# Performance work log

Measured on AMD Instinct MI355X. Metric: run time of the kernel, lower is better.

Reference implementation:

```python
import jax, jax.numpy as jnp
import numpy as np

N_NODES = 50000
N_EDGES = 800000
IN_FEATS = 128
OUT_FEATS = 128


def setup_inputs() -> dict:
    key = jax.random.key(0)
    k1, k2, k3, k4, k5, k6 = jax.random.split(key, 6)
    features = jax.random.normal(k1, (N_NODES, IN_FEATS), dtype=jnp.float32)
    norm = jax.random.uniform(k2, (N_NODES, 1), dtype=jnp.float32)
    W = jax.random.normal(k3, (OUT_FEATS, IN_FEATS), dtype=jnp.float32) * (1.0 / np.sqrt(IN_FEATS))
    b = jax.random.normal(k4, (OUT_FEATS,), dtype=jnp.float32) * 0.01
    src = jax.random.randint(k5, (N_EDGES,), 0, N_NODES, dtype=jnp.int32)
    dst = jax.random.randint(k6, (N_EDGES,), 0, N_NODES, dtype=jnp.int32)
    return {"features": features, "norm": norm, "W": W, "b": b, "src": src, "dst": dst}


def reference(features, norm, W, b, src, dst):
    # message: h_src * norm_src  -> [E, F]
    msg = features[src] * norm[src]
    # reduce: sum over incoming edges, scale by dst norm -> [N, F]
    agg = jax.ops.segment_sum(msg, dst, num_segments=N_NODES) * norm
    # node apply: linear + tanh
    h = jnp.tanh(agg @ W.T + b)
    return h
```

## Files before the change

### kernel.cpp

```cpp
#include <hip/hip_runtime.h>
#include <hip/hip_fp16.h>
#include <math.h>

#define NBITS 7
#define BNODES 128
#define CHUNK 4096
#define BSHIFT 12

typedef _Float16 half4v __attribute__((ext_vector_type(4)));
typedef _Float16 half8v __attribute__((ext_vector_type(8)));
typedef float f32x4 __attribute__((ext_vector_type(4)));

__device__ __forceinline__ unsigned hpack(float a, float b) {
  __half2 h = __floats2half2_rn(a, b);
  return *reinterpret_cast<unsigned*>(&h);
}

union FusedSmem {
  struct {
    _Float16 Wh[128][136];
    _Float16 Ah[64][136];
  } g;
  struct {
    int lcount[512];
    int lbase[512];
    int gbase[512];
    int aux[256];
    unsigned stage[CHUNK];
    int s_total;
  } p;
};

__global__ __launch_bounds__(256) void fused_kernel(
    const float* __restrict__ feat, const float* __restrict__ norm,
    const float* __restrict__ W, unsigned* __restrict__ Yh, int n_nodes,
    const int* __restrict__ src, const int* __restrict__ dst,
    int* __restrict__ cursor, unsigned* __restrict__ recs, int n_edges,
    int nb, int gblocks) {
  __shared__ __align__(16) FusedSmem sm;
  const int t = threadIdx.x;

  if ((int)blockIdx.x < gblocks) {
    const int node0 = blockIdx.x * 64;

#pragma unroll
    for (int k = 0; k < 16; ++k) {
      int e4 = k * 256 + t;
      int oo = e4 >> 5;
      int f4 = (e4 & 31) * 4;
      float4 w = *(const float4*)&W[oo * 128 + f4];
      half4v h;
      h.x = (_Float16)w.x; h.y = (_Float16)w.y;
      h.z = (_Float16)w.z; h.w = (_Float16)w.w;
      *(half4v*)&sm.g.Wh[oo][f4] = h;
    }
#pragma unroll
    for (int k = 0; k < 8; ++k) {
      int e4 = k * 256 + t;
      int nn = e4 >> 5;
      int f4 = (e4 & 31) * 4;
      int node = node0 + nn;
      float4 a = (node < n_nodes)
                     ? *(const float4*)&feat[(size_t)node * 128 + f4]
                     : make_float4(0.f, 0.f, 0.f, 0.f);
      half4v h;
      h.x = (_Float16)a.x; h.y = (_Float16)a.y;
      h.z = (_Float16)a.z; h.w = (_Float16)a.w;
      *(half4v*)&sm.g.Ah[nn][f4] = h;
    }
    __syncthreads();

    const int wv = t >> 6;
    const int l = t & 63;
    const int row16 = l & 15;
    const int kq = l >> 4;

    f32x4 acc[8];
#pragma unroll
    for (int ot = 0; ot < 8; ++ot) acc[ot] = (f32x4){0.f, 0.f, 0.f, 0.f};

#pragma unroll
    for (int ks = 0; ks < 4; ++ks) {
      half8v nfrag = *(const half8v*)&sm.g.Ah[wv * 16 + row16][kq * 8 + ks * 32];
#pragma unroll
      for (int ot = 0; ot < 8; ++ot) {
        half8v wfrag = *(const half8v*)&sm.g.Wh[ot * 16 + row16][kq * 8 + ks * 32];
        acc[ot] = __builtin_amdgcn_mfma_f32_16x16x32_f16(wfrag, nfrag, acc[ot], 0, 0, 0);
      }
    }

    int node = node0 + wv * 16 + row16;
    if (node < n_nodes) {
      float nm = norm[node];
#pragma unroll
      for (int ot = 0; ot < 8; ++ot) {
        uint2 u;
        u.x = hpack(acc[ot][0] * nm, acc[ot][1] * nm);
        u.y = hpack(acc[ot][2] * nm, acc[ot][3] * nm);
        ((uint2*)Yh)[(size_t)node * 32 + ot * 4 + kq] = u;
      }
    }
  } else {
    const int cbase = ((int)blockIdx.x - gblocks) * CHUNK;

    sm.p.lcount[t] = 0; sm.p.lcount[t + 256] = 0;
    __syncthreads();

    int es[16], ed[16], rk[16];
#pragma unroll
    for (int q = 0; q < 4; ++q) {
      int i4 = (cbase >> 2) + q * 256 + t;
      int e0 = i4 << 2;
      int4 sv, dv;
      if (e0 + 3 < n_edges) {
        sv = ((const int4*)src)[i4];
        dv = ((const int4*)dst)[i4];
      } else {
        sv.x = (e0 + 0 < n_edges) ? src[e0 + 0] : 0;
        sv.y = (e0 + 1 < n_edges) ? src[e0 + 1] : 0;
        sv.z = (e0 + 2 < n_edges) ? src[e0 + 2] : 0;
        sv.w = 0;
        dv.x = (e0 + 0 < n_edges) ? dst[e0 + 0] : -1;
        dv.y = (e0 + 1 < n_edges) ? dst[e0 + 1] : -1;
        dv.z = (e0 + 2 < n_edges) ? dst[e0 + 2] : -1;
        dv.w = -1;
      }
      es[q * 4 + 0] = sv.x; ed[q * 4 + 0] = dv.x;
      es[q * 4 + 1] = sv.y; ed[q * 4 + 1] = dv.y;
      es[q * 4 + 2] = sv.z; ed[q * 4 + 2] = dv.z;
      es[q * 4 + 3] = sv.w; ed[q * 4 + 3] = dv.w;
    }
#pragma unroll
    for (int k = 0; k < 16; ++k)
      rk[k] = (ed[k] >= 0) ? atomicAdd(&sm.p.lcount[ed[k] >> NBITS], 1) : 0;
    __syncthreads();

    int a = sm.p.lcount[2 * t] + sm.p.lcount[2 * t + 1];
    sm.p.aux[t] = a;
    __syncthreads();
    for (int off = 1; off < 256; off <<= 1) {
      int u = (t >= off) ? sm.p.aux[t - off] : 0;
      __syncthreads();
      sm.p.aux[t] += u;
      __syncthreads();
    }
    int ex = sm.p.aux[t] - a;
    sm.p.lbase[2 * t] = ex;
    sm.p.lbase[2 * t + 1] = ex + sm.p.lcount[2 * t];
    if (t == 255) sm.p.s_total = sm.p.aux[255];
    __syncthreads();

    for (int b = t; b < nb; b += 256)
      sm.p.gbase[b] = (sm.p.lcount[b] > 0)
                          ? ((b << BSHIFT) + atomicAdd(&cursor[b], sm.p.lcount[b]))
                          : 0;
    __syncthreads();

#pragma unroll
    for (int k = 0; k < 16; ++k) {
      if (ed[k] >= 0) {
        int b = ed[k] >> NBITS;
        sm.p.stage[sm.p.lbase[b] + rk[k]] = (unsigned)es[k] | ((unsigned)ed[k] << 16);
      }
    }
    __syncthreads();

    int total = sm.p.s_total;
    for (int r = t; r < total; r += 256) {
      unsigned rec = sm.p.stage[r];
      int b = (int)(rec >> (16 + NBITS));
      recs[sm.p.gbase[b] + (r - sm.p.lbase[b])] = rec;
    }
  }
}

__global__ __launch_bounds__(512) void localize_kernel(
    const unsigned* __restrict__ recs, const int* __restrict__ cursor,
    int* __restrict__ sorted_src, int* __restrict__ row_start,
    int* __restrict__ counts_d, int n_nodes) {
  __shared__ int lc[BNODES];
  __shared__ int ls[BNODES];
  __shared__ int cur[BNODES];
  const int t = threadIdx.x;
  const int b = blockIdx.x;
  const int cbeg = b << BSHIFT;
  const int cnt = cursor[b];

  if (t < BNODES) lc[t] = 0;
  __syncthreads();
  for (int i = t; i < cnt; i += 512) {
    unsigned rec = recs[cbeg + i];
    atomicAdd(&lc[(rec >> 16) & (BNODES - 1)], 1);
  }
  __syncthreads();
  if (t < BNODES) ls[t] = lc[t];
  __syncthreads();
  for (int off = 1; off < BNODES; off <<= 1) {
    int u = (t < BNODES && t >= off) ? ls[t - off] : 0;
    __syncthreads();
    if (t < BNODES) ls[t] += u;
    __syncthreads();
  }
  if (t < BNODES) {
    int ex = ls[t] - lc[t];
    cur[t] = ex;
    int node = (b << NBITS) + t;
    if (node < n_nodes) {
      counts_d[node] = lc[t];
      row_start[node] = cbeg + ex;
    }
  }
  __syncthreads();
  for (int i = t; i < cnt; i += 512) {
    unsigned rec = recs[cbeg + i];
    int nl = (rec >> 16) & (BNODES - 1);
    int p = atomicAdd(&cur[nl], 1);
    sorted_src[cbeg + p] = (int)(rec & 0xffffu);
  }
}

__global__ __launch_bounds__(256) void gather_kernel(
    const unsigned* __restrict__ Yh, const int* __restrict__ sorted_src,
    const int* __restrict__ row_start, const int* __restrict__ counts_d,
    const float* __restrict__ norm, const float* __restrict__ b,
    float* __restrict__ out, int n_nodes) {
  int node = blockIdx.x * 4 + (threadIdx.x >> 6);
  if (node >= n_nodes) return;
  int lane = threadIdx.x & 63;
  int beg = row_start[node];
  int cnt = counts_d[node];
  float accx = 0.f, accy = 0.f;

  for (int base = 0; base < cnt; base += 64) {
    int m = cnt - base;
    if (m > 64) m = 64;
    int myid = (lane < m) ? sorted_src[beg + base + lane] : 0;
    int g = 0;
    for (; g + 16 <= m; g += 16) {
      int sid[16];
      unsigned uu[16];
#pragma unroll
      for (int q = 0; q < 16; ++q) sid[q] = __builtin_amdgcn_readlane(myid, g + q);
#pragma unroll
      for (int q = 0; q < 16; ++q) uu[q] = Yh[(size_t)sid[q] * 64 + lane];
#pragma unroll
      for (int q = 0; q < 16; ++q) {
        float2 v = __half22float2(*reinterpret_cast<__half2*>(&uu[q]));
        accx += v.x;
        accy += v.y;
      }
    }
    for (; g + 8 <= m; g += 8) {
      int sid[8];
      unsigned uu[8];
#pragma unroll
      for (int q = 0; q < 8; ++q) sid[q] = __builtin_amdgcn_readlane(myid, g + q);
#pragma unroll
      for (int q = 0; q < 8; ++q) uu[q] = Yh[(size_t)sid[q] * 64 + lane];
#pragma unroll
      for (int q = 0; q < 8; ++q) {
        float2 v = __half22float2(*reinterpret_cast<__half2*>(&uu[q]));
        accx += v.x;
        accy += v.y;
      }
    }
    for (; g < m; ++g) {
      int s = __builtin_amdgcn_readlane(myid, g);
      unsigned u = Yh[(size_t)s * 64 + lane];
      float2 v = __half22float2(*reinterpret_cast<__half2*>(&u));
      accx += v.x;
      accy += v.y;
    }
  }
  float nm = norm[node];
  float2 bb = ((const float2*)b)[lane];
  float2 h;
  h.x = tanhf(accx * nm + bb.x);
  h.y = tanhf(accy * nm + bb.y);
  ((float2*)out)[(size_t)node * 64 + lane] = h;
}

extern "C" void kernel_launch(void* const* d_in, const int* in_sizes, int n_in,
                              void* d_out, int out_size, void* d_ws, size_t ws_size,
                              hipStream_t stream) {
  const float* feat = (const float*)d_in[0];
  const float* norm = (const float*)d_in[1];
  const float* W    = (const float*)d_in[2];
  const float* b    = (const float*)d_in[3];
  const int* src    = (const int*)d_in[4];
  const int* dst    = (const int*)d_in[5];
  float* out        = (float*)d_out;

  const int n_nodes = in_sizes[1];
  const int n_edges = in_sizes[4];
  const int nb = (n_nodes + BNODES - 1) / BNODES;

  char* base = (char*)d_ws;
  unsigned* Yh = (unsigned*)base;
  size_t off = (size_t)n_nodes * 64 * sizeof(unsigned);
  off = (off + 255) & ~(size_t)255;
  int* cursor = (int*)(base + off); off += (size_t)nb * 4;
  off = (off + 255) & ~(size_t)255;
  unsigned* recs = (unsigned*)(base + off); off += ((size_t)nb << BSHIFT) * 4;
  off = (off + 255) & ~(size_t)255;
  int* sorted_src = (int*)(base + off); off += ((size_t)nb << BSHIFT) * 4;
  off = (off + 255) & ~(size_t)255;
  int* row_start = (int*)(base + off); off += (size_t)n_nodes * 4;
  off = (off + 255) & ~(size_t)255;
  int* counts_d = (int*)(base + off); off += (size_t)n_nodes * 4;

  hipMemsetAsync(cursor, 0, (size_t)nb * sizeof(int), stream);

  int gblocks = (n_nodes + 63) / 64;
  int chunks = (n_edges + CHUNK - 1) / CHUNK;
  fused_kernel<<<gblocks + chunks, 256, 0, stream>>>(
      feat, norm, W, Yh, n_nodes, src, dst, cursor, recs, n_edges, nb, gblocks);

  localize_kernel<<<nb, 512, 0, stream>>>(recs, cursor, sorted_src,
                                          row_start, counts_d, n_nodes);

  int nblocks = (n_nodes + 3) / 4;
  gather_kernel<<<nblocks, 256, 0, stream>>>(Yh, sorted_src, row_start, counts_d,
                                             norm, b, out, n_nodes);
}
```

Measured before the change: 73.15 us.

## Fuse bucket localization and gather into one kernel using shared-memory CSR

The localize and gather kernels are merged into one. Each block handles half of a 128-node bucket, counting-sorts that bucket's edge records into a shared-memory list of 16-bit source ids, then aggregates fp16 rows for its 64 nodes and applies norm, bias and tanh. This drops the global sorted_src, row_start and counts arrays and one kernel launch. In exchange each block reads the bucket's records twice and discards half of them, only 782 blocks each walk 8 nodes serially per wave, and the inner unroll drops from 16 to 8 loads in flight.

```diff
diff --git a/kernel.cpp b/kernel.cpp
--- a/kernel.cpp
+++ b/kernel.cpp
@@ -174,110 +174,99 @@
   }
 }
 
-__global__ __launch_bounds__(512) void localize_kernel(
-    const unsigned* __restrict__ recs, const int* __restrict__ cursor,
-    int* __restrict__ sorted_src, int* __restrict__ row_start,
-    int* __restrict__ counts_d, int n_nodes) {
-  __shared__ int lc[BNODES];
-  __shared__ int ls[BNODES];
-  __shared__ int cur[BNODES];
+__global__ __launch_bounds__(512) void lgather_kernel(
+    const unsigned* __restrict__ Yh, const unsigned* __restrict__ recs,
+    const int* __restrict__ cursor, const float* __restrict__ norm,
+    const float* __restrict__ bias, float* __restrict__ out, int n_nodes) {
+  __shared__ int lc[64];
+  __shared__ int ls[64];
+  __shared__ int lbase[64];
+  __shared__ int cur[64];
+  __shared__ unsigned short sorted_l[1 << BSHIFT];
   const int t = threadIdx.x;
-  const int b = blockIdx.x;
+  const int b = blockIdx.x >> 1;
+  const int half = blockIdx.x & 1;
   const int cbeg = b << BSHIFT;
   const int cnt = cursor[b];
 
-  if (t < BNODES) lc[t] = 0;
-  __syncthreads();
-  for (int i = t; i < cnt; i += 512) {
-    unsigned rec = recs[cbeg + i];
-    atomicAdd(&lc[(rec >> 16) & (BNODES - 1)], 1);
-  }
-  __syncthreads();
-  if (t < BNODES) ls[t] = lc[t];
-  __syncthreads();
-  for (int off = 1; off < BNODES; off <<= 1) {
-    int u = (t < BNODES && t >= off) ? ls[t - off] : 0;
-    __syncthreads();
-    if (t < BNODES) ls[t] += u;
-    __syncthreads();
-  }
-  if (t < BNODES) {
-    int ex = ls[t] - lc[t];
-    cur[t] = ex;
-    int node = (b << NBITS) + t;
-    if (node < n_nodes) {
-      counts_d[node] = lc[t];
-      row_start[node] = cbeg + ex;
-    }
-  }
-  __syncthreads();
+  if (t < 64) lc[t] = 0;
+  __syncthreads();
+
   for (int i = t; i < cnt; i += 512) {
     unsigned rec = recs[cbeg + i];
     int nl = (rec >> 16) & (BNODES - 1);
-    int p = atomicAdd(&cur[nl], 1);
-    sorted_src[cbeg + p] = (int)(rec & 0xffffu);
-  }
-}
-
-__global__ __launch_bounds__(256) void gather_kernel(
-    const unsigned* __restrict__ Yh, const int* __restrict__ sorted_src,
-    const int* __restrict__ row_start, const int* __restrict__ counts_d,
-    const float* __restrict__ norm, const float* __restrict__ b,
-    float* __restrict__ out, int n_nodes) {
-  int node = blockIdx.x * 4 + (threadIdx.x >> 6);
-  if (node >= n_nodes) return;
-  int lane = threadIdx.x & 63;
-  int beg = row_start[node];
-  int cnt = counts_d[node];
-  float accx = 0.f, accy = 0.f;
-
-  for (int base = 0; base < cnt; base += 64) {
-    int m = cnt - base;
-    if (m > 64) m = 64;
-    int myid = (lane < m) ? sorted_src[beg + base + lane] : 0;
-    int g = 0;
-    for (; g + 16 <= m; g += 16) {
-      int sid[16];
-      unsigned uu[16];
-#pragma unroll
-      for (int q = 0; q < 16; ++q) sid[q] = __builtin_amdgcn_readlane(myid, g + q);
-#pragma unroll
-      for (int q = 0; q < 16; ++q) uu[q] = Yh[(size_t)sid[q] * 64 + lane];
-#pragma unroll
-      for (int q = 0; q < 16; ++q) {
-        float2 v = __half22float2(*reinterpret_cast<__half2*>(&uu[q]));
+    if ((nl >> 6) == half) atomicAdd(&lc[nl & 63], 1);
+  }
+  __syncthreads();
+  if (t < 64) ls[t] = lc[t];
+  __syncthreads();
+  for (int off = 1; off < 64; off <<= 1) {
+    int u = (t < 64 && t >= off) ? ls[t - off] : 0;
+    __syncthreads();
+    if (t < 64) ls[t] += u;
+    __syncthreads();
+  }
+  if (t < 64) {
+    int ex = ls[t] - lc[t];
+    lbase[t] = ex;
+    cur[t] = ex;
+  }
+  __syncthreads();
+
+  for (int i = t; i < cnt; i += 512) {
+    unsigned rec = recs[cbeg + i];
+    int nl = (rec >> 16) & (BNODES - 1);
+    if ((nl >> 6) == half) {
+      int p = atomicAdd(&cur[nl & 63], 1);
+      sorted_l[p] = (unsigned short)(rec & 0xffffu);
+    }
+  }
+  __syncthreads();
+
+  const int wv = t >> 6;
+  const int lane = t & 63;
+#pragma unroll
+  for (int j = 0; j < 8; ++j) {
+    int idx = wv * 8 + j;
+    int node = (b << NBITS) + half * 64 + idx;
+    if (node >= n_nodes) continue;
+    int beg = lbase[idx];
+    int m = lc[idx];
+    float accx = 0.f, accy = 0.f;
+    for (int base = 0; base < m; base += 64) {
+      int mm = m - base;
+      if (mm > 64) mm = 64;
+      int myid = (lane < mm) ? (int)sorted_l[beg + base + lane] : 0;
+      int g = 0;
+      for (; g + 8 <= mm; g += 8) {
+        int sid[8];
+        unsigned uu[8];
+#pragma unroll
+        for (int q = 0; q < 8; ++q) sid[q] = __builtin_amdgcn_readlane(myid, g + q);
+#pragma unroll
+        for (int q = 0; q < 8; ++q) uu[q] = Yh[(size_t)sid[q] * 64 + lane];
+#pragma unroll
+        for (int q = 0; q < 8; ++q) {
+          float2 v = __half22float2(*reinterpret_cast<__half2*>(&uu[q]));
+          accx += v.x;
+          accy += v.y;
+        }
+      }
+      for (; g < mm; ++g) {
+        int s = __builtin_amdgcn_readlane(myid, g);
+        unsigned u = Yh[(size_t)s * 64 + lane];
+        float2 v = __half22float2(*reinterpret_cast<__half2*>(&u));
         accx += v.x;
         accy += v.y;
       }
     }
-    for (; g + 8 <= m; g += 8) {
-      int sid[8];
-      unsigned uu[8];
-#pragma unroll
-      for (int q = 0; q < 8; ++q) sid[q] = __builtin_amdgcn_readlane(myid, g + q);
-#pragma unroll
-      for (int q = 0; q < 8; ++q) uu[q] = Yh[(size_t)sid[q] * 64 + lane];
-#pragma unroll
-      for (int q = 0; q < 8; ++q) {
-        float2 v = __half22float2(*reinterpret_cast<__half2*>(&uu[q]));
-        accx += v.x;
-        accy += v.y;
-      }
-    }
-    for (; g < m; ++g) {
-      int s = __builtin_amdgcn_readlane(myid, g);
-      unsigned u = Yh[(size_t)s * 64 + lane];
-      float2 v = __half22float2(*reinterpret_cast<__half2*>(&u));
-      accx += v.x;
-      accy += v.y;
-    }
-  }
-  float nm = norm[node];
-  float2 bb = ((const float2*)b)[lane];
-  float2 h;
-  h.x = tanhf(accx * nm + bb.x);
-  h.y = tanhf(accy * nm + bb.y);
-  ((float2*)out)[(size_t)node * 64 + lane] = h;
+    float nm = norm[node];
+    float2 bb = ((const float2*)bias)[lane];
+    float2 h;
+    h.x = tanhf(accx * nm + bb.x);
+    h.y = tanhf(accy * nm + bb.y);
+    ((float2*)out)[(size_t)node * 64 + lane] = h;
+  }
 }
 
 extern "C" void kernel_launch(void* const* d_in, const int* in_sizes, int n_in,
@@ -302,12 +291,6 @@
   int* cursor = (int*)(base + off); off += (size_t)nb * 4;
   off = (off + 255) & ~(size_t)255;
   unsigned* recs = (unsigned*)(base + off); off += ((size_t)nb << BSHIFT) * 4;
-  off = (off + 255) & ~(size_t)255;
-  int* sorted_src = (int*)(base + off); off += ((size_t)nb << BSHIFT) * 4;
-  off = (off + 255) & ~(size_t)255;
-  int* row_start = (int*)(base + off); off += (size_t)n_nodes * 4;
-  off = (off + 255) & ~(size_t)255;
-  int* counts_d = (int*)(base + off); off += (size_t)n_nodes * 4;
 
   hipMemsetAsync(cursor, 0, (size_t)nb * sizeof(int), stream);
 
@@ -316,10 +299,5 @@
   fused_kernel<<<gblocks + chunks, 256, 0, stream>>>(
       feat, norm, W, Yh, n_nodes, src, dst, cursor, recs, n_edges, nb, gblocks);
 
-  localize_kernel<<<nb, 512, 0, stream>>>(recs, cursor, sorted_src,
-                                          row_start, counts_d, n_nodes);
-
-  int nblocks = (n_nodes + 3) / 4;
-  gather_kernel<<<nblocks, 256, 0, stream>>>(Yh, sorted_src, row_start, counts_d,
-                                             norm, b, out, n_nodes);
+  lgather_kernel<<<nb * 2, 512, 0, stream>>>(Yh, recs, cursor, norm, b, out, n_nodes);
 }
```

After: 69.56 us. 1.05x faster.
